# Kernel optimization log

Measured on AMD Instinct MI355X. Metric: run time of the kernel, lower is better.

The kernel has to match this reference:

```python
import jax, jax.numpy as jnp
import numpy as np
import math

N_LAYER = 4
D = 1024
H = 16
V = 32000
MAX_LEN = 2048
B = 2
L = 2048
EPS = 1e-6


def positional_encoding(max_len, dim):
    pos = jnp.arange(max_len, dtype=jnp.float32)[:, None]
    div = jnp.exp(jnp.arange(0, dim, 2, dtype=jnp.float32) * (-math.log(10000.0) / dim))
    ang = pos * div  # [max_len, dim//2]
    pe = jnp.zeros((max_len, dim), dtype=jnp.float32)
    pe = pe.at[:, 0::2].set(jnp.sin(ang)).at[:, 1::2].set(jnp.cos(ang))
    return pe


def setup_inputs() -> dict:
    key = jax.random.key(0)
    ks = jax.random.split(key, 20)
    s = 0.02
    inp = {
        "input_ids": jax.random.randint(ks[0], (B, L), 0, V),
        "embed": jax.random.normal(ks[1], (V, D), jnp.float32) * s,
        "Wq": jax.random.normal(ks[2], (N_LAYER, D, D), jnp.float32) * s,
        "bq": jnp.zeros((N_LAYER, D), jnp.float32),
        "Wk": jax.random.normal(ks[3], (N_LAYER, D, D), jnp.float32) * s,
        "bk": jnp.zeros((N_LAYER, D), jnp.float32),
        "Wv": jax.random.normal(ks[4], (N_LAYER, D, D), jnp.float32) * s,
        "bv": jnp.zeros((N_LAYER, D), jnp.float32),
        "Wo": jax.random.normal(ks[5], (N_LAYER, D, D), jnp.float32) * s,
        "bo": jnp.zeros((N_LAYER, D), jnp.float32),
        "Wproj": jax.random.normal(ks[6], (N_LAYER, D, 2 * D), jnp.float32) * s,
        "bproj": jnp.zeros((N_LAYER, 2 * D), jnp.float32),
        "Wup": jax.random.normal(ks[7], (N_LAYER, D, 2 * D), jnp.float32) * s,
        "bup": jnp.zeros((N_LAYER, 2 * D), jnp.float32),
        "Wdown": jax.random.normal(ks[8], (N_LAYER, 2 * D, D), jnp.float32) * s,
        "bdown": jnp.zeros((N_LAYER, D), jnp.float32),
        "gammas": jnp.ones((2 * N_LAYER, D), jnp.float32),
        "Wlogits": jax.random.normal(ks[9], (D, V), jnp.float32) * s,
        "blogits": jnp.zeros((V,), jnp.float32),
    }
    return inp


def rmsnorm(x, gamma):
    ms = jnp.mean(x * x, axis=-1, keepdims=True)
    return x * jax.lax.rsqrt(ms + EPS) * gamma


def attention(x, Wq, bq, Wk, bk, Wv, bv, Wo, bo):
    b, l, d = x.shape
    dh = d // H
    q = (x @ Wq + bq).reshape(b, l, H, dh)
    k = (x @ Wk + bk).reshape(b, l, H, dh)
    v = (x @ Wv + bv).reshape(b, l, H, dh)
    scores = jnp.einsum("blhd,bmhd->bhlm", q, k) / math.sqrt(dh)
    causal = jnp.tril(jnp.ones((l, l), dtype=bool))  # True where allowed
    scores = jnp.where(causal, scores, -jnp.inf)
    attn = jax.nn.softmax(scores, axis=-1)
    out = jnp.einsum("bhlm,bmhd->blhd", attn, v).reshape(b, l, d)
    return out @ Wo + bo


def ffn(x, Wproj, bproj, Wup, bup, Wdown, bdown):
    proj = x @ Wproj + bproj
    up = x @ Wup + bup
    gate = jax.nn.silu(proj * up)
    return gate @ Wdown + bdown


def reference(input_ids, embed, Wq, bq, Wk, bk, Wv, bv, Wo, bo,
              Wproj, bproj, Wup, bup, Wdown, bdown, gammas, Wlogits, blogits):
    b, l = input_ids.shape
    pe = positional_encoding(MAX_LEN, D)[:l]
    x = embed[input_ids] + pe
    for i in range(N_LAYER):
        x = x + attention(rmsnorm(x, gammas[2 * i]),
                          Wq[i], bq[i], Wk[i], bk[i], Wv[i], bv[i], Wo[i], bo[i])
        x = x + ffn(rmsnorm(x, gammas[2 * i + 1]),
                    Wproj[i], bproj[i], Wup[i], bup[i], Wdown[i], bdown[i])
    return x @ Wlogits + blogits
```

## Files before the change

kernel.cpp:

```cpp
#include <hip/hip_runtime.h>


typedef _Float16 f16;
typedef _Float16 v8h __attribute__((ext_vector_type(8)));
typedef float    v4f __attribute__((ext_vector_type(4)));

#define B_   2
#define L_   2048
#define D_   1024
#define H_   16
#define V_   32000
#define M_   (B_ * L_)

__device__ inline void g2l16(const void* g, void* l) {
  __builtin_amdgcn_global_load_lds((const __attribute__((address_space(1))) void*)g,
                                   (__attribute__((address_space(3))) void*)l,
                                   16, 0, 0);
}

__device__ inline void tile_map(int& m, int& n) {
  const int GX = (int)gridDim.x, GY = (int)gridDim.y;
  const int nwg = GX * GY;
  const int flat = (int)(blockIdx.y * gridDim.x + blockIdx.x);
  const int per = nwg >> 3, r = nwg & 7;
  const int xcd = flat & 7, lo = flat >> 3;
  const int swz = (xcd < r ? xcd * (per + 1) : r * (per + 1) + (xcd - r) * per) + lo;
  const int MG = 4;
  const int band = swz / (MG * GY), rem = swz % (MG * GY);
  n = rem / MG;
  m = band * MG + (rem % MG);
}

template<int EPI>
__global__ __launch_bounds__(256, 2) void gemm_wt(
    const f16* __restrict__ A, const f16* __restrict__ Bt,
    const float* __restrict__ bias, const float* resid, void* outp,
    int N, int K)
{
  __shared__ alignas(16) f16 As[256 * 32];
  __shared__ alignas(16) f16 Bs[128 * 32];

  int bm, bn;
  tile_map(bm, bn);

  const int tid  = threadIdx.x;
  const int wave = tid >> 6, lane = tid & 63;
  const int quad = lane >> 4, l16 = lane & 15;
  const long tm = (long)bm * 256;
  const long tn = (long)bn * 128;
  const int wm = (wave >> 1) * 128, wn = (wave & 1) * 64;

  v4f acc[8][4];
  for (int i = 0; i < 8; ++i)
    for (int j = 0; j < 4; ++j)
      for (int r = 0; r < 4; ++r) acc[i][j][r] = 0.f;

  for (int k0 = 0; k0 < K; k0 += 32) {
    __syncthreads();
    for (int h = 0; h < 4; ++h) {
      int c = h * 256 + tid;
      long row = c >> 2;
      int jslot = c & 3;
      long koff = (long)k0 + ((jslot ^ ((row >> 1) & 3)) << 3);
      g2l16(A + (tm + row) * K + koff, As + (h * 256 + wave * 64) * 8);
    }
    for (int h = 0; h < 2; ++h) {
      int c = h * 256 + tid;
      long row = c >> 2;
      int jslot = c & 3;
      long koff = (long)k0 + ((jslot ^ ((row >> 1) & 3)) << 3);
      g2l16(Bt + (tn + row) * K + koff, Bs + (h * 256 + wave * 64) * 8);
    }
    __syncthreads();

    v8h a[8], b[4];
    for (int i = 0; i < 8; ++i) {
      int arow = wm + i * 16 + l16;
      a[i] = *(const v8h*)(As + arow * 32 + ((quad ^ ((arow >> 1) & 3)) << 3));
    }
    for (int j = 0; j < 4; ++j) {
      int brow = wn + j * 16 + l16;
      b[j] = *(const v8h*)(Bs + brow * 32 + ((quad ^ ((brow >> 1) & 3)) << 3));
    }
    for (int i = 0; i < 8; ++i)
      for (int j = 0; j < 4; ++j)
        acc[i][j] = __builtin_amdgcn_mfma_f32_16x16x32_f16(a[i], b[j], acc[i][j], 0, 0, 0);
  }

  for (int i = 0; i < 8; ++i)
    for (int r = 0; r < 4; ++r) {
      long row = tm + wm + i * 16 + quad * 4 + r;
      for (int j = 0; j < 4; ++j) {
        long col = tn + wn + j * 16 + l16;
        float v = acc[i][j][r] + bias[col];
        long idx = row * (long)N + col;
        if (EPI == 0)      ((f16*)outp)[idx] = (f16)v;
        else if (EPI == 1) ((float*)outp)[idx] = resid[idx] + v;
        else               ((float*)outp)[idx] = v;
      }
    }
}

template<int EPI>
__global__ __launch_bounds__(256) void gemm64_bt(
    const f16* __restrict__ A, const f16* __restrict__ Bt,
    const float* __restrict__ bias, const float* resid, void* outp,
    int N, int K)
{
  __shared__ alignas(16) f16 As[128 * 32];
  __shared__ alignas(16) f16 Bs[64 * 32];

  int bm, bn;
  tile_map(bm, bn);

  const int tid  = threadIdx.x;
  const int wave = tid >> 6, lane = tid & 63;
  const int quad = lane >> 4, l16 = lane & 15;
  const long tm = (long)bm * 128;
  const long tn = (long)bn * 64;
  const int wm = (wave >> 1) * 64, wn = (wave & 1) * 32;

  v4f acc[4][2];
  for (int i = 0; i < 4; ++i)
    for (int j = 0; j < 2; ++j)
      for (int r = 0; r < 4; ++r) acc[i][j][r] = 0.f;

  for (int k0 = 0; k0 < K; k0 += 32) {
    __syncthreads();
    for (int h = 0; h < 2; ++h) {
      int c = h * 256 + tid;
      long row = c >> 2;
      int jslot = c & 3;
      long koff = (long)k0 + ((jslot ^ ((row >> 1) & 3)) << 3);
      g2l16(A + (tm + row) * K + koff, As + (h * 256 + wave * 64) * 8);
    }
    {
      int c = tid;
      long row = c >> 2;
      int jslot = c & 3;
      long koff = (long)k0 + ((jslot ^ ((row >> 1) & 3)) << 3);
      g2l16(Bt + (tn + row) * K + koff, Bs + (wave * 64) * 8);
    }
    __syncthreads();

    v8h a[4], b[2];
    for (int i = 0; i < 4; ++i) {
      int arow = wm + i * 16 + l16;
      a[i] = *(const v8h*)(As + arow * 32 + ((quad ^ ((arow >> 1) & 3)) << 3));
    }
    for (int j = 0; j < 2; ++j) {
      int brow = wn + j * 16 + l16;
      b[j] = *(const v8h*)(Bs + brow * 32 + ((quad ^ ((brow >> 1) & 3)) << 3));
    }
    for (int i = 0; i < 4; ++i)
      for (int j = 0; j < 2; ++j)
        acc[i][j] = __builtin_amdgcn_mfma_f32_16x16x32_f16(a[i], b[j], acc[i][j], 0, 0, 0);
  }

  for (int i = 0; i < 4; ++i)
    for (int r = 0; r < 4; ++r) {
      long row = tm + wm + i * 16 + quad * 4 + r;
      for (int j = 0; j < 2; ++j) {
        long col = tn + wn + j * 16 + l16;
        float v = acc[i][j][r] + bias[col];
        long idx = row * (long)N + col;
        if (EPI == 0)      ((f16*)outp)[idx] = (f16)v;
        else if (EPI == 1) ((float*)outp)[idx] = resid[idx] + v;
        else               ((float*)outp)[idx] = v;
      }
    }
}

__global__ __launch_bounds__(256) void attn_k(const f16* __restrict__ qkv,
                                              f16* __restrict__ attno)
{
  const int qt = (int)gridDim.x - 1 - blockIdx.x;
  const int bh = blockIdx.y;
  const int b = bh >> 4, h = bh & 15;
  const int tid = threadIdx.x;
  const int wave = tid >> 6, lane = tid & 63;
  const int quad = lane >> 4, l16 = lane & 15;

  __shared__ alignas(16) f16 Ks[64 * 64];
  __shared__ alignas(16) f16 Vt[64 * 64];
  __shared__ alignas(16) f16 Ps[4][16 * 64];

  const f16* base = qkv + (size_t)b * L_ * 3072 + h * 64;

  const int qrow = qt * 64 + wave * 16 + l16;
  const v8h qf0 = *(const v8h*)(base + (size_t)qrow * 3072 + quad * 8);
  const v8h qf1 = *(const v8h*)(base + (size_t)qrow * 3072 + 32 + quad * 8);

  v4f of[4];
  float m_i[4], l_i[4];
  for (int n = 0; n < 4; ++n)
    for (int r = 0; r < 4; ++r) of[n][r] = 0.f;
  for (int r = 0; r < 4; ++r) { m_i[r] = -1e30f; l_i[r] = 0.f; }

  const int nblocks = qt + 1;

  for (int kb = 0; kb < nblocks; ++kb) {
    const int key0 = kb * 64;
    __syncthreads();
    for (int h2 = 0; h2 < 2; ++h2) {
      int c = h2 * 256 + tid;
      int row = c >> 3, jslot = c & 7;
      const f16* ksrc = base + 1024 + (size_t)(key0 + row) * 3072
                        + ((jslot ^ (row & 7)) << 3);
      g2l16(ksrc, Ks + (h2 * 256 + wave * 64) * 8);
    }
    for (int h2 = 0; h2 < 2; ++h2) {
      int key = tid >> 2;
      int dc = (tid & 3) + h2 * 4;
      const f16* vsrc = base + 2048 + (size_t)(key0 + key) * 3072 + dc * 8;
      v8h vv = *(const v8h*)vsrc;
      for (int e = 0; e < 8; ++e) {
        int d = dc * 8 + e;
        Vt[d * 64 + (((key >> 3) ^ (d & 7)) << 3) + (key & 7)] = vv[e];
      }
    }
    __syncthreads();

    v4f sf[4];
    for (int s = 0; s < 4; ++s)
      for (int r = 0; r < 4; ++r) sf[s][r] = 0.f;
    for (int s = 0; s < 4; ++s) {
      int krow = s * 16 + l16;
      v8h kf0 = *(const v8h*)(Ks + krow * 64 + ((quad       ^ (krow & 7)) << 3));
      v8h kf1 = *(const v8h*)(Ks + krow * 64 + (((4 + quad) ^ (krow & 7)) << 3));
      sf[s] = __builtin_amdgcn_mfma_f32_16x16x32_f16(qf0, kf0, sf[s], 0, 0, 0);
      sf[s] = __builtin_amdgcn_mfma_f32_16x16x32_f16(qf1, kf1, sf[s], 0, 0, 0);
    }

    const int qg0 = qt * 64 + wave * 16 + quad * 4;
    float pv[4][4];
    for (int s = 0; s < 4; ++s)
      for (int r = 0; r < 4; ++r) {
        float sc = sf[s][r] * 0.125f;
        int kg = key0 + s * 16 + l16;
        if (kg > qg0 + r) sc = -1e30f;
        pv[s][r] = sc;
      }

    for (int r = 0; r < 4; ++r) {
      float mx = fmaxf(fmaxf(pv[0][r], pv[1][r]), fmaxf(pv[2][r], pv[3][r]));
      for (int o = 8; o; o >>= 1) mx = fmaxf(mx, __shfl_xor(mx, o, 64));
      float mnew = fmaxf(m_i[r], mx);
      float alpha = expf(m_i[r] - mnew);
      m_i[r] = mnew;
      float rs = 0.f;
      for (int s = 0; s < 4; ++s) {
        pv[s][r] = expf(pv[s][r] - mnew);
        rs += pv[s][r];
      }
      for (int o = 8; o; o >>= 1) rs += __shfl_xor(rs, o, 64);
      l_i[r] = l_i[r] * alpha + rs;
      for (int n = 0; n < 4; ++n) of[n][r] *= alpha;
      int qr = quad * 4 + r;
      for (int s = 0; s < 4; ++s) {
        int key = s * 16 + l16;
        Ps[wave][qr * 64 + ((((key >> 3)) ^ (qr & 7)) << 3) + (key & 7)]
            = (f16)pv[s][r];
      }
    }
    __syncthreads();

    v8h pf0 = *(const v8h*)(&Ps[wave][0] + l16 * 64 + ((quad       ^ (l16 & 7)) << 3));
    v8h pf1 = *(const v8h*)(&Ps[wave][0] + l16 * 64 + (((4 + quad) ^ (l16 & 7)) << 3));
    for (int n = 0; n < 4; ++n) {
      int d = n * 16 + l16;
      v8h vf0 = *(const v8h*)(Vt + d * 64 + ((quad       ^ (d & 7)) << 3));
      v8h vf1 = *(const v8h*)(Vt + d * 64 + (((4 + quad) ^ (d & 7)) << 3));
      of[n] = __builtin_amdgcn_mfma_f32_16x16x32_f16(pf0, vf0, of[n], 0, 0, 0);
      of[n] = __builtin_amdgcn_mfma_f32_16x16x32_f16(pf1, vf1, of[n], 0, 0, 0);
    }
  }

  const int q = qt * 64 + wave * 16 + quad * 4;
  f16* orow = attno + (size_t)b * L_ * 1024 + h * 64;
  for (int r = 0; r < 4; ++r) {
    float inv = 1.0f / l_i[r];
    for (int n = 0; n < 4; ++n)
      orow[(size_t)(q + r) * 1024 + n * 16 + l16] = (f16)(of[n][r] * inv);
  }
}

__global__ __launch_bounds__(256) void embed_pe(const int* __restrict__ ids,
                                                const float* __restrict__ emb,
                                                float* __restrict__ x)
{
  const int bl = blockIdx.x;
  const int l = bl & (L_ - 1);
  const int id = ids[bl];
  const float* e = emb + (size_t)id * D_;
  float* xr = x + (size_t)bl * D_;
  const int d0 = threadIdx.x * 4;
  for (int i = 0; i < 4; ++i) {
    int d = d0 + i;
    int p = d >> 1;
    float ang = (float)l * expf((float)(2 * p) * -0.008994473019508053f);
    float pe = (d & 1) ? cosf(ang) : sinf(ang);
    xr[d] = e[d] + pe;
  }
}

__global__ __launch_bounds__(256) void rmsnorm_k(const float* __restrict__ x,
                                                 const float* __restrict__ gamma,
                                                 f16* __restrict__ y)
{
  const int row = blockIdx.x;
  const float4 v = ((const float4*)(x + (size_t)row * D_))[threadIdx.x];
  float s = v.x * v.x + v.y * v.y + v.z * v.z + v.w * v.w;
  for (int o = 32; o; o >>= 1) s += __shfl_xor(s, o, 64);
  __shared__ float red[4];
  const int wave = threadIdx.x >> 6;
  if ((threadIdx.x & 63) == 0) red[wave] = s;
  __syncthreads();
  const float tot = red[0] + red[1] + red[2] + red[3];
  const float scale = rsqrtf(tot * (1.0f / D_) + 1e-6f);
  f16* yr = y + (size_t)row * D_;
  const int d = threadIdx.x * 4;
  yr[d]     = (f16)(v.x * scale * gamma[d]);
  yr[d + 1] = (f16)(v.y * scale * gamma[d + 1]);
  yr[d + 2] = (f16)(v.z * scale * gamma[d + 2]);
  yr[d + 3] = (f16)(v.w * scale * gamma[d + 3]);
}

__global__ __launch_bounds__(256) void transpose_cvt(const float* __restrict__ in,
                                                     f16* __restrict__ out,
                                                     int K, int N)
{
  __shared__ float tile[32][33];
  const int r = threadIdx.x >> 5, c = threadIdx.x & 31;
  const size_t bk = (size_t)blockIdx.y * 32;
  const size_t bn = (size_t)blockIdx.x * 32;
  for (int i = 0; i < 32; i += 8)
    tile[r + i][c] = in[(bk + r + i) * N + bn + c];
  __syncthreads();
  for (int i = 0; i < 32; i += 8)
    out[(bn + r + i) * K + bk + c] = (f16)tile[c][r + i];
}

__global__ __launch_bounds__(256) void gate_k(const f16* __restrict__ PU,
                                              f16* __restrict__ g)
{
  const int e = (blockIdx.x * 256 + threadIdx.x) * 4;
  const int row = e >> 11, col = e & 2047;
  const f16* p = PU + (size_t)row * 4096 + col;
  const f16* u = p + 2048;
  f16* go = g + (size_t)row * 2048 + col;
  for (int i = 0; i < 4; ++i) {
    float z = (float)p[i] * (float)u[i];
    go[i] = (f16)(z / (1.0f + expf(-z)));
  }
}

__global__ __launch_bounds__(256) void cast_k(const float* __restrict__ x,
                                              f16* __restrict__ y)
{
  const int i = blockIdx.x * 1024 + threadIdx.x * 4;
  const float4 v = *(const float4*)(x + i);
  y[i] = (f16)v.x; y[i + 1] = (f16)v.y; y[i + 2] = (f16)v.z; y[i + 3] = (f16)v.w;
}

__global__ __launch_bounds__(256) void build_biases(
    const float* bq, const float* bk, const float* bv,
    const float* bp, const float* bu, float* bqkv, float* bpu)
{
  const int i = blockIdx.x;
  for (int j = threadIdx.x; j < 3072; j += 256)
    bqkv[i * 3072 + j] = j < 1024 ? bq[i * 1024 + j]
                       : j < 2048 ? bk[i * 1024 + j - 1024]
                                  : bv[i * 1024 + j - 2048];
  for (int j = threadIdx.x; j < 4096; j += 256)
    bpu[i * 4096 + j] = j < 2048 ? bp[i * 2048 + j] : bu[i * 2048 + j - 2048];
}

extern "C" void kernel_launch(void* const* d_in, const int* in_sizes, int n_in,
                              void* d_out, int out_size, void* d_ws, size_t ws_size,
                              hipStream_t stream)
{
  (void)in_sizes; (void)n_in; (void)out_size; (void)ws_size;
  const int*   ids     = (const int*)  d_in[0];
  const float* embed   = (const float*)d_in[1];
  const float* Wq      = (const float*)d_in[2];
  const float* bq      = (const float*)d_in[3];
  const float* Wk      = (const float*)d_in[4];
  const float* bk      = (const float*)d_in[5];
  const float* Wv      = (const float*)d_in[6];
  const float* bv      = (const float*)d_in[7];
  const float* Wo      = (const float*)d_in[8];
  const float* bo      = (const float*)d_in[9];
  const float* Wproj   = (const float*)d_in[10];
  const float* bproj   = (const float*)d_in[11];
  const float* Wup     = (const float*)d_in[12];
  const float* bup     = (const float*)d_in[13];
  const float* Wdown   = (const float*)d_in[14];
  const float* bdown   = (const float*)d_in[15];
  const float* gammas  = (const float*)d_in[16];
  const float* Wlogits = (const float*)d_in[17];
  const float* blogits = (const float*)d_in[18];

  char* ws = (char*)d_ws;
  float* x    = (float*)ws;
  f16*   y    = (f16*)  (ws + 16777216);
  float* bqkv = (float*)(ws + 25165824);
  float* bpu  = (float*)(ws + 25214976);
  f16*   wbuf = (f16*)  (ws + 25280512);
  f16* wqkvT  = wbuf;
  f16* woT    = wbuf + 3145728;
  f16* wpuT   = wbuf + 4194304;
  f16* wdownT = wbuf + 8388608;

  char* ob  = (char*)d_out;
  f16* qkv   = (f16*)ob;
  f16* attno = (f16*)(ob + 25165824);
  f16* PU    = (f16*)(ob + 33554432);
  f16* g     = (f16*)(ob + 67108864);

  embed_pe<<<M_, 256, 0, stream>>>(ids, embed, x);
  build_biases<<<4, 256, 0, stream>>>(bq, bk, bv, bproj, bup, bqkv, bpu);

  for (int i = 0; i < 4; ++i) {
    const float* Wqi = Wq + (size_t)i * 1048576;
    const float* Wki = Wk + (size_t)i * 1048576;
    const float* Wvi = Wv + (size_t)i * 1048576;
    const float* Woi = Wo + (size_t)i * 1048576;
    const float* Wpi = Wproj + (size_t)i * 2097152;
    const float* Wui = Wup   + (size_t)i * 2097152;
    const float* Wdi = Wdown + (size_t)i * 2097152;

    transpose_cvt<<<dim3(32, 32), 256, 0, stream>>>(Wqi, wqkvT,                1024, 1024);
    transpose_cvt<<<dim3(32, 32), 256, 0, stream>>>(Wki, wqkvT + 1048576,      1024, 1024);
    transpose_cvt<<<dim3(32, 32), 256, 0, stream>>>(Wvi, wqkvT + 2097152,      1024, 1024);
    transpose_cvt<<<dim3(32, 32), 256, 0, stream>>>(Woi, woT,                  1024, 1024);
    transpose_cvt<<<dim3(64, 32), 256, 0, stream>>>(Wpi, wpuT,                 1024, 2048);
    transpose_cvt<<<dim3(64, 32), 256, 0, stream>>>(Wui, wpuT + 2097152,       1024, 2048);
    transpose_cvt<<<dim3(32, 64), 256, 0, stream>>>(Wdi, wdownT,               2048, 1024);

    rmsnorm_k<<<M_, 256, 0, stream>>>(x, gammas + (size_t)(2 * i) * 1024, y);
    gemm_wt<0><<<dim3(16, 24), 256, 0, stream>>>(y, wqkvT, bqkv + i * 3072, nullptr, qkv, 3072, 1024);
    attn_k<<<dim3(32, 32), 256, 0, stream>>>(qkv, attno);
    gemm64_bt<1><<<dim3(32, 16), 256, 0, stream>>>(attno, woT, bo + i * 1024, x, x, 1024, 1024);

    rmsnorm_k<<<M_, 256, 0, stream>>>(x, gammas + (size_t)(2 * i + 1) * 1024, y);
    gemm_wt<0><<<dim3(16, 32), 256, 0, stream>>>(y, wpuT, bpu + i * 4096, nullptr, PU, 4096, 1024);
    gate_k<<<8192, 256, 0, stream>>>(PU, g);
    gemm64_bt<1><<<dim3(32, 16), 256, 0, stream>>>(g, wdownT, bdown + i * 1024, x, x, 1024, 2048);
  }

  transpose_cvt<<<dim3(1000, 32), 256, 0, stream>>>(Wlogits, wbuf, 1024, 32000);
  cast_k<<<M_, 256, 0, stream>>>(x, y);
  gemm_wt<2><<<dim3(16, 250), 256, 0, stream>>>(y, wbuf, blogits, nullptr, (float*)d_out, 32000, 1024);
}
```

Measured before the change: 2.527 ms.

## Double-buffer GEMM LDS tiles with async global-to-LDS prefetch two tiles ahead

Both GEMM kernels switch to double-buffered LDS tiles. Global-to-LDS loads for tile t+2 are issued while MFMA work runs on the current tile, with vmcnt waits and barriers replacing the two __syncthreads per iteration. Address computation is hoisted out of the k-loop and the MFMA block is wrapped in s_setprio. This is meant to hide global memory latency behind compute, at the cost of doubled LDS use (48KB for the large tile), which may reduce occupancy from the 2-blocks-per-CU target.

```diff
diff --git a/kernel.cpp b/kernel.cpp
--- a/kernel.cpp
+++ b/kernel.cpp
@@ -37,8 +37,8 @@
     const float* __restrict__ bias, const float* resid, void* outp,
     int N, int K)
 {
-  __shared__ alignas(16) f16 As[256 * 32];
-  __shared__ alignas(16) f16 Bs[128 * 32];
+  __shared__ alignas(16) f16 As[2][256 * 32];
+  __shared__ alignas(16) f16 Bs[2][128 * 32];
 
   int bm, bn;
   tile_map(bm, bn);
@@ -50,46 +50,93 @@
   const long tn = (long)bn * 128;
   const int wm = (wave >> 1) * 128, wn = (wave & 1) * 64;
 
+  const f16* asrc[4];
+  const f16* bsrc[2];
+  #pragma unroll
+  for (int h = 0; h < 4; ++h) {
+    int c = h * 256 + tid;
+    long row = c >> 2;
+    int jslot = c & 3;
+    asrc[h] = A + (tm + row) * K + ((jslot ^ ((row >> 1) & 3)) << 3);
+  }
+  #pragma unroll
+  for (int h = 0; h < 2; ++h) {
+    int c = h * 256 + tid;
+    long row = c >> 2;
+    int jslot = c & 3;
+    bsrc[h] = Bt + (tn + row) * K + ((jslot ^ ((row >> 1) & 3)) << 3);
+  }
+  int aoff[8], boff[4];
+  #pragma unroll
+  for (int i = 0; i < 8; ++i) {
+    int arow = wm + i * 16 + l16;
+    aoff[i] = arow * 32 + ((quad ^ ((arow >> 1) & 3)) << 3);
+  }
+  #pragma unroll
+  for (int j = 0; j < 4; ++j) {
+    int brow = wn + j * 16 + l16;
+    boff[j] = brow * 32 + ((quad ^ ((brow >> 1) & 3)) << 3);
+  }
+
   v4f acc[8][4];
+  #pragma unroll
   for (int i = 0; i < 8; ++i)
+    #pragma unroll
     for (int j = 0; j < 4; ++j)
+      #pragma unroll
       for (int r = 0; r < 4; ++r) acc[i][j][r] = 0.f;
 
-  for (int k0 = 0; k0 < K; k0 += 32) {
-    __syncthreads();
-    for (int h = 0; h < 4; ++h) {
-      int c = h * 256 + tid;
-      long row = c >> 2;
-      int jslot = c & 3;
-      long koff = (long)k0 + ((jslot ^ ((row >> 1) & 3)) << 3);
-      g2l16(A + (tm + row) * K + koff, As + (h * 256 + wave * 64) * 8);
-    }
-    for (int h = 0; h < 2; ++h) {
-      int c = h * 256 + tid;
-      long row = c >> 2;
-      int jslot = c & 3;
-      long koff = (long)k0 + ((jslot ^ ((row >> 1) & 3)) << 3);
-      g2l16(Bt + (tn + row) * K + koff, Bs + (h * 256 + wave * 64) * 8);
-    }
-    __syncthreads();
-
+  const int nt = K >> 5;
+
+#define STAGE_WT(buf, t)                                                   \
+  {                                                                        \
+    const long ko_ = (long)(t) << 5;                                       \
+    _Pragma("unroll")                                                      \
+    for (int h_ = 0; h_ < 4; ++h_)                                         \
+      g2l16(asrc[h_] + ko_, As[buf] + (h_ * 256 + wave * 64) * 8);         \
+    _Pragma("unroll")                                                      \
+    for (int h_ = 0; h_ < 2; ++h_)                                         \
+      g2l16(bsrc[h_] + ko_, Bs[buf] + (h_ * 256 + wave * 64) * 8);         \
+  }
+
+  STAGE_WT(0, 0)
+  STAGE_WT(1, 1)
+  asm volatile("s_waitcnt vmcnt(6)" ::: "memory");
+  __builtin_amdgcn_s_barrier();
+
+  int cur = 0;
+  for (int t = 0; t < nt; ++t) {
     v8h a[8], b[4];
-    for (int i = 0; i < 8; ++i) {
-      int arow = wm + i * 16 + l16;
-      a[i] = *(const v8h*)(As + arow * 32 + ((quad ^ ((arow >> 1) & 3)) << 3));
-    }
-    for (int j = 0; j < 4; ++j) {
-      int brow = wn + j * 16 + l16;
-      b[j] = *(const v8h*)(Bs + brow * 32 + ((quad ^ ((brow >> 1) & 3)) << 3));
-    }
+    #pragma unroll
+    for (int i = 0; i < 8; ++i) a[i] = *(const v8h*)(As[cur] + aoff[i]);
+    #pragma unroll
+    for (int j = 0; j < 4; ++j) b[j] = *(const v8h*)(Bs[cur] + boff[j]);
+    __builtin_amdgcn_s_setprio(1);
+    #pragma unroll
     for (int i = 0; i < 8; ++i)
+      #pragma unroll
       for (int j = 0; j < 4; ++j)
         acc[i][j] = __builtin_amdgcn_mfma_f32_16x16x32_f16(a[i], b[j], acc[i][j], 0, 0, 0);
-  }
-
+    __builtin_amdgcn_s_setprio(0);
+    __builtin_amdgcn_sched_barrier(0);
+    __builtin_amdgcn_s_barrier();
+    if (t + 2 < nt) {
+      STAGE_WT(cur, t + 2)
+      asm volatile("s_waitcnt vmcnt(6)" ::: "memory");
+    } else {
+      asm volatile("s_waitcnt vmcnt(0)" ::: "memory");
+    }
+    __builtin_amdgcn_sched_barrier(0);
+    __builtin_amdgcn_s_barrier();
+    cur ^= 1;
+  }
+
+  #pragma unroll
   for (int i = 0; i < 8; ++i)
+    #pragma unroll
     for (int r = 0; r < 4; ++r) {
       long row = tm + wm + i * 16 + quad * 4 + r;
+      #pragma unroll
       for (int j = 0; j < 4; ++j) {
         long col = tn + wn + j * 16 + l16;
         float v = acc[i][j][r] + bias[col];
@@ -99,6 +146,7 @@
         else               ((float*)outp)[idx] = v;
       }
     }
+#undef STAGE_WT
 }
 
 template<int EPI>
@@ -107,8 +155,8 @@
     const float* __restrict__ bias, const float* resid, void* outp,
     int N, int K)
 {
-  __shared__ alignas(16) f16 As[128 * 32];
-  __shared__ alignas(16) f16 Bs[64 * 32];
+  __shared__ alignas(16) f16 As[2][128 * 32];
+  __shared__ alignas(16) f16 Bs[2][64 * 32];
 
   int bm, bn;
   tile_map(bm, bn);
@@ -120,46 +168,90 @@
   const long tn = (long)bn * 64;
   const int wm = (wave >> 1) * 64, wn = (wave & 1) * 32;
 
+  const f16* asrc[2];
+  const f16* bsrc;
+  #pragma unroll
+  for (int h = 0; h < 2; ++h) {
+    int c = h * 256 + tid;
+    long row = c >> 2;
+    int jslot = c & 3;
+    asrc[h] = A + (tm + row) * K + ((jslot ^ ((row >> 1) & 3)) << 3);
+  }
+  {
+    int c = tid;
+    long row = c >> 2;
+    int jslot = c & 3;
+    bsrc = Bt + (tn + row) * K + ((jslot ^ ((row >> 1) & 3)) << 3);
+  }
+  int aoff[4], boff[2];
+  #pragma unroll
+  for (int i = 0; i < 4; ++i) {
+    int arow = wm + i * 16 + l16;
+    aoff[i] = arow * 32 + ((quad ^ ((arow >> 1) & 3)) << 3);
+  }
+  #pragma unroll
+  for (int j = 0; j < 2; ++j) {
+    int brow = wn + j * 16 + l16;
+    boff[j] = brow * 32 + ((quad ^ ((brow >> 1) & 3)) << 3);
+  }
+
   v4f acc[4][2];
+  #pragma unroll
   for (int i = 0; i < 4; ++i)
+    #pragma unroll
     for (int j = 0; j < 2; ++j)
+      #pragma unroll
       for (int r = 0; r < 4; ++r) acc[i][j][r] = 0.f;
 
-  for (int k0 = 0; k0 < K; k0 += 32) {
-    __syncthreads();
-    for (int h = 0; h < 2; ++h) {
-      int c = h * 256 + tid;
-      long row = c >> 2;
-      int jslot = c & 3;
-      long koff = (long)k0 + ((jslot ^ ((row >> 1) & 3)) << 3);
-      g2l16(A + (tm + row) * K + koff, As + (h * 256 + wave * 64) * 8);
-    }
-    {
-      int c = tid;
-      long row = c >> 2;
-      int jslot = c & 3;
-      long koff = (long)k0 + ((jslot ^ ((row >> 1) & 3)) << 3);
-      g2l16(Bt + (tn + row) * K + koff, Bs + (wave * 64) * 8);
-    }
-    __syncthreads();
-
+  const int nt = K >> 5;
+
+#define STAGE_64(buf, t)                                                   \
+  {                                                                        \
+    const long ko_ = (long)(t) << 5;                                       \
+    _Pragma("unroll")                                                      \
+    for (int h_ = 0; h_ < 2; ++h_)                                         \
+      g2l16(asrc[h_] + ko_, As[buf] + (h_ * 256 + wave * 64) * 8);         \
+    g2l16(bsrc + ko_, Bs[buf] + (wave * 64) * 8);                          \
+  }
+
+  STAGE_64(0, 0)
+  STAGE_64(1, 1)
+  asm volatile("s_waitcnt vmcnt(3)" ::: "memory");
+  __builtin_amdgcn_s_barrier();
+
+  int cur = 0;
+  for (int t = 0; t < nt; ++t) {
     v8h a[4], b[2];
-    for (int i = 0; i < 4; ++i) {
-      int arow = wm + i * 16 + l16;
-      a[i] = *(const v8h*)(As + arow * 32 + ((quad ^ ((arow >> 1) & 3)) << 3));
-    }
-    for (int j = 0; j < 2; ++j) {
-      int brow = wn + j * 16 + l16;
-      b[j] = *(const v8h*)(Bs + brow * 32 + ((quad ^ ((brow >> 1) & 3)) << 3));
-    }
+    #pragma unroll
+    for (int i = 0; i < 4; ++i) a[i] = *(const v8h*)(As[cur] + aoff[i]);
+    #pragma unroll
+    for (int j = 0; j < 2; ++j) b[j] = *(const v8h*)(Bs[cur] + boff[j]);
+    __builtin_amdgcn_s_setprio(1);
+    #pragma unroll
     for (int i = 0; i < 4; ++i)
+      #pragma unroll
       for (int j = 0; j < 2; ++j)
         acc[i][j] = __builtin_amdgcn_mfma_f32_16x16x32_f16(a[i], b[j], acc[i][j], 0, 0, 0);
-  }
-
+    __builtin_amdgcn_s_setprio(0);
+    __builtin_amdgcn_sched_barrier(0);
+    __builtin_amdgcn_s_barrier();
+    if (t + 2 < nt) {
+      STAGE_64(cur, t + 2)
+      asm volatile("s_waitcnt vmcnt(3)" ::: "memory");
+    } else {
+      asm volatile("s_waitcnt vmcnt(0)" ::: "memory");
+    }
+    __builtin_amdgcn_sched_barrier(0);
+    __builtin_amdgcn_s_barrier();
+    cur ^= 1;
+  }
+
+  #pragma unroll
   for (int i = 0; i < 4; ++i)
+    #pragma unroll
     for (int r = 0; r < 4; ++r) {
       long row = tm + wm + i * 16 + quad * 4 + r;
+      #pragma unroll
       for (int j = 0; j < 2; ++j) {
         long col = tn + wn + j * 16 + l16;
         float v = acc[i][j][r] + bias[col];
@@ -169,6 +261,7 @@
         else               ((float*)outp)[idx] = v;
       }
     }
+#undef STAGE_64
 }
 
 __global__ __launch_bounds__(256) void attn_k(const f16* __restrict__ qkv,
```

New measurement: 2.500 ms. About the same (-1.1%).
